# Kernel optimization log

Hardware: AMD Instinct MI355X
Metric: run time of the kernel (lower is better)

## Reference

```python
import jax, jax.numpy as jnp
import numpy as np

N_NODES, N_EDGES, N_GRAPHS, N_FEATS = 100000, 1600000, 256, 128
BN_EPS = 1e-5


def setup_inputs() -> dict:
    key = jax.random.key(0)
    ks = jax.random.split(key, 12)
    x = jax.random.normal(ks[0], (N_NODES, N_FEATS), jnp.float32)
    edge_index = jax.random.randint(ks[1], (2, N_EDGES), 0, N_NODES, dtype=jnp.int64)
    batch = jnp.sort(jax.random.randint(ks[2], (N_NODES,), 0, N_GRAPHS, dtype=jnp.int64))
    s = 0.05
    return {
        "x": x,
        "edge_index": edge_index,
        "batch": batch,
        "W1": jax.random.normal(ks[3], (N_FEATS, 32), jnp.float32) * s,
        "b1": jnp.zeros((32,), jnp.float32),
        "W2": jax.random.normal(ks[4], (32, 64), jnp.float32) * s,
        "b2": jnp.zeros((64,), jnp.float32),
        "fcW1": jax.random.normal(ks[5], (64, 32), jnp.float32) * s,
        "fcb1": jnp.zeros((32,), jnp.float32),
        "gamma": jnp.ones((32,), jnp.float32),
        "beta": jnp.zeros((32,), jnp.float32),
        "fcW2": jax.random.normal(ks[6], (32, 1), jnp.float32) * s,
        "fcb2": jnp.zeros((1,), jnp.float32),
    }


def _gcn_conv(x, src, dst, deg_inv, W, b):
    # PyG GCNConv: h = x @ W; out[d] = sum_e norm_e * h[src_e] + self-loop + b
    h = x @ W  # [N, out]
    norm = deg_inv[src] * deg_inv[dst]  # [E]
    msg = h[src] * norm[:, None]
    out = jax.ops.segment_sum(msg, dst, num_segments=x.shape[0])
    out = out + (deg_inv * deg_inv)[:, None] * h  # self-loop contribution
    return out + b


def reference(x, edge_index, batch, W1, b1, W2, b2, fcW1, fcb1, gamma, beta, fcW2, fcb2):
    src, dst = edge_index[0], edge_index[1]
    n = x.shape[0]
    # degree with self loops, computed on target nodes (PyG default)
    deg = 1.0 + jax.ops.segment_sum(jnp.ones_like(src, dtype=x.dtype), dst, num_segments=n)
    deg_inv = jax.lax.rsqrt(deg)
    h = _gcn_conv(x, src, dst, deg_inv, W1, b1)   # [N, 32]
    h = _gcn_conv(h, src, dst, deg_inv, W2, b2)   # [N, 64]
    # scatter_mean over graph batch
    sums = jax.ops.segment_sum(h, batch, num_segments=N_GRAPHS)  # [G, 64]
    cnt = jax.ops.segment_sum(jnp.ones((n,), h.dtype), batch, num_segments=N_GRAPHS)
    pooled = sums / jnp.maximum(cnt, 1.0)[:, None]
    # head: Linear -> ReLU -> BatchNorm1d (batch stats) -> Dropout(eval=id) -> Linear -> Softplus
    z = jax.nn.relu(pooled @ fcW1 + fcb1)  # [G, 32]
    mu = jnp.mean(z, axis=0)
    var = jnp.var(z, axis=0)
    z = (z - mu) * jax.lax.rsqrt(var + BN_EPS) * gamma + beta
    out = jax.nn.softplus(z @ fcW2 + fcb2)  # [G, 1]
    return out
```

## Files before the change

kernel.cpp:

```cpp
#include <hip/hip_runtime.h>

#define NN 100000
#define NE 1600000
#define NG 256

#define BSH 8
#define NPB 256
#define NBKT ((NN + NPB - 1) / NPB)
#define STRIDE 4608
#define TILE 8192
#define NB_P1 ((NE + TILE - 1) / TILE)

__device__ __forceinline__ unsigned short f2bf(float x) {
    unsigned int u = __float_as_uint(x);
    u += 0x7FFFu + ((u >> 16) & 1u);
    return (unsigned short)(u >> 16);
}
__device__ __forceinline__ float2 bf2x2(unsigned int v) {
    float2 r;
    r.x = __uint_as_float(v << 16);
    r.y = __uint_as_float(v & 0xFFFF0000u);
    return r;
}
__device__ __forceinline__ unsigned int bfpack(float x, float y) {
    return (unsigned int)f2bf(x) | ((unsigned int)f2bf(y) << 16);
}

__global__ __launch_bounds__(1024) void part_kernel(const int* __restrict__ src,
                                                    const int* __restrict__ dst,
                                                    int* __restrict__ bkt_cur,
                                                    int* __restrict__ epack) {
    __shared__ int hist[512];
    __shared__ int scan0[512];
    __shared__ int cur[NBKT];
    __shared__ int gbase[NBKT];
    __shared__ int stage[TILE];
    __shared__ unsigned short sb[TILE];
    int tid = threadIdx.x;
    int e0 = blockIdx.x * TILE;
    int e1 = min(e0 + TILE, NE);
    int n = e1 - e0;

    for (int i = tid; i < 512; i += 1024) hist[i] = 0;
    __syncthreads();

    int d_[8], s_[8];
#pragma unroll
    for (int k = 0; k < 8; ++k) {
        int e = e0 + tid + k * 1024;
        if (e < e1) {
            d_[k] = dst[e];
            s_[k] = src[e];
            atomicAdd(&hist[d_[k] >> BSH], 1);
        }
    }
    __syncthreads();

    if (tid < 512) scan0[tid] = hist[tid];
    __syncthreads();
    for (int off = 1; off < 512; off <<= 1) {
        int t = (tid < 512 && tid >= off) ? scan0[tid - off] : 0;
        __syncthreads();
        if (tid < 512) scan0[tid] += t;
        __syncthreads();
    }
    if (tid < NBKT) {
        int h = hist[tid];
        int ex = scan0[tid] - h;
        cur[tid] = ex;
        gbase[tid] = tid * STRIDE + (h ? atomicAdd(&bkt_cur[tid], h) : 0) - ex;
    }
    __syncthreads();

#pragma unroll
    for (int k = 0; k < 8; ++k) {
        int e = e0 + tid + k * 1024;
        if (e < e1) {
            int d = d_[k];
            int bk = d >> BSH;
            int p = atomicAdd(&cur[bk], 1);
            stage[p] = s_[k] | ((d & (NPB - 1)) << 17);
            sb[p] = (unsigned short)bk;
        }
    }
    __syncthreads();

    for (int j = tid; j < n; j += 1024) {
        int bk = sb[j];
        int a = gbase[bk] + j;
        if (a < (bk + 1) * STRIDE)
            epack[a] = stage[j];
    }
}

__global__ __launch_bounds__(512) void build_kernel(const int* __restrict__ epack,
                                                    const int* __restrict__ bkt_cur,
                                                    int* __restrict__ row_beg,
                                                    int* __restrict__ row_deg,
                                                    int* __restrict__ col,
                                                    float* __restrict__ deg_inv) {
    __shared__ int cnt[NPB];
    __shared__ int ts[NPB];
    int b = blockIdx.x;
    int tid = threadIdx.x;
    int ebase = b * STRIDE;
    int eend = ebase + min(bkt_cur[b], STRIDE);
    int nbase = b << BSH;
    if (tid < NPB) cnt[tid] = 0;
    __syncthreads();
    for (int e = ebase + tid; e < eend; e += 512)
        atomicAdd(&cnt[epack[e] >> 17], 1);
    __syncthreads();
    int v = 0;
    if (tid < NPB) {
        v = cnt[tid];
        ts[tid] = v;
    }
    __syncthreads();
    for (int off = 1; off < NPB; off <<= 1) {
        int t = (tid < NPB && tid >= off) ? ts[tid - off] : 0;
        __syncthreads();
        if (tid < NPB) ts[tid] += t;
        __syncthreads();
    }
    if (tid < NPB) {
        int loff = ts[tid] - v;
        int node = nbase + tid;
        if (node < NN) {
            row_beg[node] = ebase + loff;
            row_deg[node] = v;
            deg_inv[node] = rsqrtf(1.0f + (float)v);
        }
        cnt[tid] = loff;
    }
    __syncthreads();
    for (int e = ebase + tid; e < eend; e += 512) {
        int rec = epack[e];
        int r = atomicAdd(&cnt[rec >> 17], 1);
        col[ebase + r] = rec & 0x1FFFF;
    }
}

__global__ __launch_bounds__(256) void gemm_x_w1(const float* __restrict__ x,
                                                 const float* __restrict__ W,
                                                 const float* __restrict__ deg_inv,
                                                 unsigned short* __restrict__ h, int N) {
    __shared__ float wsh[128 * 32];
    __shared__ float xs[32][132];
    int tid = threadIdx.x;
    int row0 = blockIdx.x * 32;
    for (int i = tid; i < 1024; i += 256)
        ((float4*)wsh)[i] = ((const float4*)W)[i];
    for (int i = tid; i < 1024; i += 256) {
        int r = i >> 5, c4 = i & 31;
        *(float4*)&xs[r][c4 * 4] = ((const float4*)(x + (size_t)(row0 + r) * 128))[c4];
    }
    __syncthreads();
    int r = tid >> 3;
    int c8 = (tid & 7) * 4;
    float acc0 = 0.f, acc1 = 0.f, acc2 = 0.f, acc3 = 0.f;
#pragma unroll
    for (int k0 = 0; k0 < 128; k0 += 4) {
        float4 xv = *(const float4*)&xs[r][k0];
#pragma unroll
        for (int j = 0; j < 4; ++j) {
            float xk = (&xv.x)[j];
            float4 wv = *(const float4*)&wsh[(k0 + j) * 32 + c8];
            acc0 += xk * wv.x;
            acc1 += xk * wv.y;
            acc2 += xk * wv.z;
            acc3 += xk * wv.w;
        }
    }
    float di = deg_inv[row0 + r];
    ushort4 o;
    o.x = f2bf(acc0 * di);
    o.y = f2bf(acc1 * di);
    o.z = f2bf(acc2 * di);
    o.w = f2bf(acc3 * di);
    *(ushort4*)&h[(size_t)(row0 + r) * 32 + c8] = o;
}

template <int MODE>
__global__ __launch_bounds__(256) void conv_bf_kernel(const int* __restrict__ row_beg,
                                                      const int* __restrict__ row_deg,
                                                      const int* __restrict__ col,
                                                      const uint2* __restrict__ h2,
                                                      const float* __restrict__ deg_inv,
                                                      const float* __restrict__ b,
                                                      uint2* __restrict__ out_bf,
                                                      const int* __restrict__ batch,
                                                      float* __restrict__ gsum,
                                                      float* __restrict__ gcnt) {
    __shared__ float sacc[2][32];
    __shared__ float scnt[2];
    __shared__ int sg[2];
    int tid = threadIdx.x;
    int gid = blockIdx.x * 256 + tid;
    int node = gid >> 3;
    int L = gid & 7;
    if (MODE == 1) {
        if (tid < 64) sacc[tid >> 5][tid & 31] = 0.f;
        if (tid < 2) scnt[tid] = 0.f;
        if (tid == 0) {
            sg[0] = batch[(size_t)blockIdx.x * 32];
            sg[1] = batch[(size_t)blockIdx.x * 32 + 31];
        }
    }
    int beg = row_beg[node];
    int end = beg + row_deg[node];
    uint2 sv = h2[node * 8 + L];
    float2 s0 = bf2x2(sv.x), s1 = bf2x2(sv.y);
    float a00 = s0.x, a01 = s0.y, a02 = s1.x, a03 = s1.y;
    float a10 = 0.f, a11 = 0.f, a12 = 0.f, a13 = 0.f;
    float a20 = 0.f, a21 = 0.f, a22 = 0.f, a23 = 0.f;
    float a30 = 0.f, a31 = 0.f, a32 = 0.f, a33 = 0.f;
    for (int j0 = beg; j0 < end; j0 += 8) {
        int idx = j0 + L;
        int myc = (idx < end) ? col[idx] : 0;
        int m = end - j0;
        if (m > 8) m = 8;
        int t = 0;
        for (; t + 4 <= m; t += 4) {
            int c0 = __shfl(myc, t, 8);
            int c1 = __shfl(myc, t + 1, 8);
            int c2 = __shfl(myc, t + 2, 8);
            int c3 = __shfl(myc, t + 3, 8);
            uint2 v0 = h2[c0 * 8 + L];
            uint2 v1 = h2[c1 * 8 + L];
            uint2 v2 = h2[c2 * 8 + L];
            uint2 v3 = h2[c3 * 8 + L];
            float2 p0 = bf2x2(v0.x), q0 = bf2x2(v0.y);
            float2 p1 = bf2x2(v1.x), q1 = bf2x2(v1.y);
            float2 p2 = bf2x2(v2.x), q2 = bf2x2(v2.y);
            float2 p3 = bf2x2(v3.x), q3 = bf2x2(v3.y);
            a00 += p0.x; a01 += p0.y; a02 += q0.x; a03 += q0.y;
            a10 += p1.x; a11 += p1.y; a12 += q1.x; a13 += q1.y;
            a20 += p2.x; a21 += p2.y; a22 += q2.x; a23 += q2.y;
            a30 += p3.x; a31 += p3.y; a32 += q3.x; a33 += q3.y;
        }
        for (; t < m; ++t) {
            int c = __shfl(myc, t, 8);
            uint2 v = h2[c * 8 + L];
            float2 p = bf2x2(v.x), q = bf2x2(v.y);
            a00 += p.x; a01 += p.y; a02 += q.x; a03 += q.y;
        }
    }
    float c0 = (a00 + a10) + (a20 + a30);
    float c1 = (a01 + a11) + (a21 + a31);
    float c2 = (a02 + a12) + (a22 + a32);
    float c3 = (a03 + a13) + (a23 + a33);
    float di = deg_inv[node];
    if (MODE == 0) {
        float o0 = di * di * c0 + di * b[4 * L];
        float o1 = di * di * c1 + di * b[4 * L + 1];
        float o2 = di * di * c2 + di * b[4 * L + 2];
        float o3 = di * di * c3 + di * b[4 * L + 3];
        out_bf[node * 8 + L] = make_uint2(bfpack(o0, o1), bfpack(o2, o3));
    } else {
        float o0 = di * c0, o1 = di * c1, o2 = di * c2, o3 = di * c3;
        __syncthreads();
        int gn = batch[node];
        int base = 4 * L;
        if (gn == sg[0]) {
            atomicAdd(&sacc[0][base + 0], o0);
            atomicAdd(&sacc[0][base + 1], o1);
            atomicAdd(&sacc[0][base + 2], o2);
            atomicAdd(&sacc[0][base + 3], o3);
            if (L == 0) atomicAdd(&scnt[0], 1.f);
        } else if (gn == sg[1]) {
            atomicAdd(&sacc[1][base + 0], o0);
            atomicAdd(&sacc[1][base + 1], o1);
            atomicAdd(&sacc[1][base + 2], o2);
            atomicAdd(&sacc[1][base + 3], o3);
            if (L == 0) atomicAdd(&scnt[1], 1.f);
        } else {
            unsafeAtomicAdd(&gsum[gn * 32 + base + 0], o0);
            unsafeAtomicAdd(&gsum[gn * 32 + base + 1], o1);
            unsafeAtomicAdd(&gsum[gn * 32 + base + 2], o2);
            unsafeAtomicAdd(&gsum[gn * 32 + base + 3], o3);
            if (L == 0) unsafeAtomicAdd(&gcnt[gn], 1.f);
        }
        __syncthreads();
        if (tid < 64) {
            int s = tid >> 5, f = tid & 31;
            if (s == 0 || sg[1] != sg[0])
                unsafeAtomicAdd(&gsum[sg[s] * 32 + f], sacc[s][f]);
        }
        if (tid == 0) unsafeAtomicAdd(&gcnt[sg[0]], scnt[0]);
        if (tid == 1 && sg[1] != sg[0]) unsafeAtomicAdd(&gcnt[sg[1]], scnt[1]);
    }
}

__global__ __launch_bounds__(256) void head_kernel(const float* __restrict__ gsum,
                                                   const float* __restrict__ gcnt,
                                                   const float* __restrict__ W2,
                                                   const float* __restrict__ b2,
                                                   const float* __restrict__ fcW1,
                                                   const float* __restrict__ fcb1,
                                                   const float* __restrict__ gamma,
                                                   const float* __restrict__ beta,
                                                   const float* __restrict__ fcW2,
                                                   const float* __restrict__ fcb2,
                                                   float* __restrict__ out) {
    __shared__ float zs[NG][33];
    __shared__ float wcs[32 * 32];
    __shared__ float bcs[32];
    __shared__ float part1[8][32];
    __shared__ float part2[8][32];
    __shared__ float mu[32], rstd[32];
    int g = threadIdx.x;

    for (int idx = g; idx < 32 * 32; idx += 256) {
        int k = idx / 32, ch = idx % 32;
        float a = 0.f;
#pragma unroll
        for (int j = 0; j < 64; ++j) a += W2[k * 64 + j] * fcW1[j * 32 + ch];
        wcs[idx] = a;
    }
    if (g < 32) {
        float a = fcb1[g];
#pragma unroll
        for (int j = 0; j < 64; ++j) a += b2[j] * fcW1[j * 32 + g];
        bcs[g] = a;
    }
    __syncthreads();

    float p32[32];
    float inv = 1.0f / fmaxf(gcnt[g], 1.0f);
    {
        const float4* gs4 = (const float4*)(gsum + g * 32);
#pragma unroll
        for (int q = 0; q < 8; ++q) {
            float4 v = gs4[q];
            p32[q * 4 + 0] = v.x * inv;
            p32[q * 4 + 1] = v.y * inv;
            p32[q * 4 + 2] = v.z * inv;
            p32[q * 4 + 3] = v.w * inv;
        }
    }
#pragma unroll 4
    for (int ch = 0; ch < 32; ++ch) {
        float acc = bcs[ch];
#pragma unroll
        for (int k = 0; k < 32; ++k) acc += p32[k] * wcs[k * 32 + ch];
        zs[g][ch] = fmaxf(acc, 0.f);
    }
    __syncthreads();

    {
        int ch = g & 31, seg = g >> 5;
        float s = 0.f, sq = 0.f;
#pragma unroll
        for (int i = 0; i < 32; ++i) {
            float v = zs[seg * 32 + i][ch];
            s += v;
            sq += v * v;
        }
        part1[seg][ch] = s;
        part2[seg][ch] = sq;
    }
    __syncthreads();
    if (g < 32) {
        float s = 0.f, sq = 0.f;
#pragma unroll
        for (int i = 0; i < 8; ++i) { s += part1[i][g]; sq += part2[i][g]; }
        float m = s / NG;
        float v = sq / NG - m * m;
        mu[g] = m;
        rstd[g] = rsqrtf(fmaxf(v, 0.f) + 1e-5f);
    }
    __syncthreads();

    float acc = fcb2[0];
#pragma unroll 4
    for (int ch = 0; ch < 32; ++ch) {
        float zn = (zs[g][ch] - mu[ch]) * rstd[ch] * gamma[ch] + beta[ch];
        acc += zn * fcW2[ch];
    }
    out[g] = fmaxf(acc, 0.f) + log1pf(expf(-fabsf(acc)));
}

extern "C" void kernel_launch(void* const* d_in, const int* in_sizes, int n_in,
                              void* d_out, int out_size, void* d_ws, size_t ws_size,
                              hipStream_t stream) {
    const float* x     = (const float*)d_in[0];
    const int*   ei    = (const int*)d_in[1];
    const int*   batch = (const int*)d_in[2];
    const float* W1    = (const float*)d_in[3];
    const float* b1    = (const float*)d_in[4];
    const float* W2    = (const float*)d_in[5];
    const float* b2    = (const float*)d_in[6];
    const float* fcW1  = (const float*)d_in[7];
    const float* fcb1  = (const float*)d_in[8];
    const float* gamma = (const float*)d_in[9];
    const float* beta  = (const float*)d_in[10];
    const float* fcW2  = (const float*)d_in[11];
    const float* fcb2  = (const float*)d_in[12];
    float* out = (float*)d_out;

    char* p = (char*)d_ws;
    int*   bkt_cur = (int*)p;        p += 400 * 4;
    float* gsum    = (float*)p;      p += (size_t)NG * 32 * 4;
    float* gcnt    = (float*)p;      p += (size_t)NG * 4;
    float* deg_inv = (float*)p;      p += (size_t)NN * 4;
    int*   row_beg = (int*)p;        p += (size_t)(NN + 8) * 4;
    int*   row_deg = (int*)p;        p += (size_t)(NN + 8) * 4;
    int*   epack   = (int*)p;        p += (size_t)NBKT * STRIDE * 4;
    int*   col     = (int*)p;        p += (size_t)NBKT * STRIDE * 4;
    unsigned short* h1s = (unsigned short*)p;  p += (size_t)NN * 32 * 2;
    uint2*          t1  = (uint2*)p;           p += (size_t)NN * 8 * 8;

    const int* srcv = ei;
    const int* dstv = ei + NE;

    hipMemsetAsync(bkt_cur, 0, 400 * 4 + (size_t)NG * 32 * 4 + (size_t)NG * 4, stream);

    part_kernel<<<NB_P1, 1024, 0, stream>>>(srcv, dstv, bkt_cur, epack);
    build_kernel<<<NBKT, 512, 0, stream>>>(epack, bkt_cur, row_beg, row_deg, col, deg_inv);

    gemm_x_w1<<<NN / 32, 256, 0, stream>>>(x, W1, deg_inv, h1s, NN);
    conv_bf_kernel<0><<<((size_t)NN * 8 + 255) / 256, 256, 0, stream>>>(
        row_beg, row_deg, col, (const uint2*)h1s, deg_inv, b1, t1, nullptr, nullptr, nullptr);

    conv_bf_kernel<1><<<((size_t)NN * 8 + 255) / 256, 256, 0, stream>>>(
        row_beg, row_deg, col, (const uint2*)t1, deg_inv, b1, nullptr, batch, gsum, gcnt);

    head_kernel<<<1, 256, 0, stream>>>(gsum, gcnt, W2, b2, fcW1, fcb1, gamma, beta, fcW2, fcb2, out);
}
```

Baseline: 227.1 us.

## Replace CSR build and pull convolution with bucketed push aggregation in shared memory

Removes the build_kernel that sorted each destination bucket into CSR rows. Degrees now come from global atomics in the partition kernel, and each convolution runs one 1024-thread block per 256-node bucket, accumulating neighbor features into a shared-memory tile with LDS atomics. The block then applies the self-loop, normalization and bias. This saves a kernel launch and the col/row arrays, but relies on heavy shared-memory float atomics and on only about 391 blocks, which may underfill the GPU.

New measurement: 893.4 us. 3.93x slower.

```diff
diff --git a/kernel.cpp b/kernel.cpp
--- a/kernel.cpp
+++ b/kernel.cpp
@@ -29,7 +29,8 @@
 __global__ __launch_bounds__(1024) void part_kernel(const int* __restrict__ src,
                                                     const int* __restrict__ dst,
                                                     int* __restrict__ bkt_cur,
-                                                    int* __restrict__ epack) {
+                                                    int* __restrict__ epack,
+                                                    int* __restrict__ deg) {
     __shared__ int hist[512];
     __shared__ int scan0[512];
     __shared__ int cur[NBKT];
@@ -87,63 +88,17 @@
 
     for (int j = tid; j < n; j += 1024) {
         int bk = sb[j];
+        int rec = stage[j];
         int a = gbase[bk] + j;
         if (a < (bk + 1) * STRIDE)
-            epack[a] = stage[j];
-    }
-}
-
-__global__ __launch_bounds__(512) void build_kernel(const int* __restrict__ epack,
-                                                    const int* __restrict__ bkt_cur,
-                                                    int* __restrict__ row_beg,
-                                                    int* __restrict__ row_deg,
-                                                    int* __restrict__ col,
-                                                    float* __restrict__ deg_inv) {
-    __shared__ int cnt[NPB];
-    __shared__ int ts[NPB];
-    int b = blockIdx.x;
-    int tid = threadIdx.x;
-    int ebase = b * STRIDE;
-    int eend = ebase + min(bkt_cur[b], STRIDE);
-    int nbase = b << BSH;
-    if (tid < NPB) cnt[tid] = 0;
-    __syncthreads();
-    for (int e = ebase + tid; e < eend; e += 512)
-        atomicAdd(&cnt[epack[e] >> 17], 1);
-    __syncthreads();
-    int v = 0;
-    if (tid < NPB) {
-        v = cnt[tid];
-        ts[tid] = v;
-    }
-    __syncthreads();
-    for (int off = 1; off < NPB; off <<= 1) {
-        int t = (tid < NPB && tid >= off) ? ts[tid - off] : 0;
-        __syncthreads();
-        if (tid < NPB) ts[tid] += t;
-        __syncthreads();
-    }
-    if (tid < NPB) {
-        int loff = ts[tid] - v;
-        int node = nbase + tid;
-        if (node < NN) {
-            row_beg[node] = ebase + loff;
-            row_deg[node] = v;
-            deg_inv[node] = rsqrtf(1.0f + (float)v);
-        }
-        cnt[tid] = loff;
-    }
-    __syncthreads();
-    for (int e = ebase + tid; e < eend; e += 512) {
-        int rec = epack[e];
-        int r = atomicAdd(&cnt[rec >> 17], 1);
-        col[ebase + r] = rec & 0x1FFFF;
+            epack[a] = rec;
+        atomicAdd(&deg[(bk << BSH) + (rec >> 17)], 1);
     }
 }
 
 __global__ __launch_bounds__(256) void gemm_x_w1(const float* __restrict__ x,
                                                  const float* __restrict__ W,
-                                                 const float* __restrict__ deg_inv,
+                                                 const int* __restrict__ deg,
                                                  unsigned short* __restrict__ h, int N) {
     __shared__ float wsh[128 * 32];
     __shared__ float xs[32][132];
@@ -172,7 +127,7 @@
             acc3 += xk * wv.w;
         }
     }
-    float di = deg_inv[row0 + r];
+    float di = rsqrtf(1.0f + (float)deg[row0 + r]);
     ushort4 o;
     o.x = f2bf(acc0 * di);
     o.y = f2bf(acc1 * di);
@@ -182,105 +137,119 @@
 }
 
 template <int MODE>
-__global__ __launch_bounds__(256) void conv_bf_kernel(const int* __restrict__ row_beg,
-                                                      const int* __restrict__ row_deg,
-                                                      const int* __restrict__ col,
-                                                      const uint2* __restrict__ h2,
-                                                      const float* __restrict__ deg_inv,
-                                                      const float* __restrict__ b,
-                                                      uint2* __restrict__ out_bf,
-                                                      const int* __restrict__ batch,
-                                                      float* __restrict__ gsum,
-                                                      float* __restrict__ gcnt) {
+__global__ __launch_bounds__(1024) void push_conv(const int* __restrict__ epack,
+                                                  const int* __restrict__ bkt_cur,
+                                                  const uint2* __restrict__ h2,
+                                                  const int* __restrict__ deg,
+                                                  const float* __restrict__ bias,
+                                                  uint2* __restrict__ out_bf,
+                                                  const int* __restrict__ batch,
+                                                  float* __restrict__ gsum,
+                                                  float* __restrict__ gcnt) {
+    __shared__ float acc[NPB * 32];
     __shared__ float sacc[2][32];
     __shared__ float scnt[2];
     __shared__ int sg[2];
+    int bk = blockIdx.x;
     int tid = threadIdx.x;
-    int gid = blockIdx.x * 256 + tid;
-    int node = gid >> 3;
-    int L = gid & 7;
+    int ebase = bk * STRIDE;
+    int ecnt = min(bkt_cur[bk], STRIDE);
+    int nbase = bk << BSH;
+
+    for (int i = tid; i < NPB * 32; i += 1024) acc[i] = 0.f;
     if (MODE == 1) {
         if (tid < 64) sacc[tid >> 5][tid & 31] = 0.f;
         if (tid < 2) scnt[tid] = 0.f;
         if (tid == 0) {
-            sg[0] = batch[(size_t)blockIdx.x * 32];
-            sg[1] = batch[(size_t)blockIdx.x * 32 + 31];
-        }
-    }
-    int beg = row_beg[node];
-    int end = beg + row_deg[node];
-    uint2 sv = h2[node * 8 + L];
-    float2 s0 = bf2x2(sv.x), s1 = bf2x2(sv.y);
-    float a00 = s0.x, a01 = s0.y, a02 = s1.x, a03 = s1.y;
-    float a10 = 0.f, a11 = 0.f, a12 = 0.f, a13 = 0.f;
-    float a20 = 0.f, a21 = 0.f, a22 = 0.f, a23 = 0.f;
-    float a30 = 0.f, a31 = 0.f, a32 = 0.f, a33 = 0.f;
-    for (int j0 = beg; j0 < end; j0 += 8) {
-        int idx = j0 + L;
-        int myc = (idx < end) ? col[idx] : 0;
-        int m = end - j0;
-        if (m > 8) m = 8;
-        int t = 0;
-        for (; t + 4 <= m; t += 4) {
-            int c0 = __shfl(myc, t, 8);
-            int c1 = __shfl(myc, t + 1, 8);
-            int c2 = __shfl(myc, t + 2, 8);
-            int c3 = __shfl(myc, t + 3, 8);
-            uint2 v0 = h2[c0 * 8 + L];
-            uint2 v1 = h2[c1 * 8 + L];
-            uint2 v2 = h2[c2 * 8 + L];
-            uint2 v3 = h2[c3 * 8 + L];
-            float2 p0 = bf2x2(v0.x), q0 = bf2x2(v0.y);
-            float2 p1 = bf2x2(v1.x), q1 = bf2x2(v1.y);
-            float2 p2 = bf2x2(v2.x), q2 = bf2x2(v2.y);
-            float2 p3 = bf2x2(v3.x), q3 = bf2x2(v3.y);
-            a00 += p0.x; a01 += p0.y; a02 += q0.x; a03 += q0.y;
-            a10 += p1.x; a11 += p1.y; a12 += q1.x; a13 += q1.y;
-            a20 += p2.x; a21 += p2.y; a22 += q2.x; a23 += q2.y;
-            a30 += p3.x; a31 += p3.y; a32 += q3.x; a33 += q3.y;
-        }
-        for (; t < m; ++t) {
-            int c = __shfl(myc, t, 8);
-            uint2 v = h2[c * 8 + L];
-            float2 p = bf2x2(v.x), q = bf2x2(v.y);
-            a00 += p.x; a01 += p.y; a02 += q.x; a03 += q.y;
-        }
-    }
-    float c0 = (a00 + a10) + (a20 + a30);
-    float c1 = (a01 + a11) + (a21 + a31);
-    float c2 = (a02 + a12) + (a22 + a32);
-    float c3 = (a03 + a13) + (a23 + a33);
-    float di = deg_inv[node];
-    if (MODE == 0) {
-        float o0 = di * di * c0 + di * b[4 * L];
-        float o1 = di * di * c1 + di * b[4 * L + 1];
-        float o2 = di * di * c2 + di * b[4 * L + 2];
-        float o3 = di * di * c3 + di * b[4 * L + 3];
-        out_bf[node * 8 + L] = make_uint2(bfpack(o0, o1), bfpack(o2, o3));
-    } else {
-        float o0 = di * c0, o1 = di * c1, o2 = di * c2, o3 = di * c3;
-        __syncthreads();
-        int gn = batch[node];
-        int base = 4 * L;
-        if (gn == sg[0]) {
-            atomicAdd(&sacc[0][base + 0], o0);
-            atomicAdd(&sacc[0][base + 1], o1);
-            atomicAdd(&sacc[0][base + 2], o2);
-            atomicAdd(&sacc[0][base + 3], o3);
-            if (L == 0) atomicAdd(&scnt[0], 1.f);
-        } else if (gn == sg[1]) {
-            atomicAdd(&sacc[1][base + 0], o0);
-            atomicAdd(&sacc[1][base + 1], o1);
-            atomicAdd(&sacc[1][base + 2], o2);
-            atomicAdd(&sacc[1][base + 3], o3);
-            if (L == 0) atomicAdd(&scnt[1], 1.f);
+            sg[0] = batch[nbase];
+            sg[1] = batch[min(nbase + NPB - 1, NN - 1)];
+        }
+    }
+    __syncthreads();
+
+    int g = tid >> 3, L = tid & 7;
+    int e = g;
+    for (; e + 384 < ecnt; e += 512) {
+        int rec0 = epack[ebase + e];
+        int rec1 = epack[ebase + e + 128];
+        int rec2 = epack[ebase + e + 256];
+        int rec3 = epack[ebase + e + 384];
+        uint2 v0 = h2[(rec0 & 0x1FFFF) * 8 + L];
+        uint2 v1 = h2[(rec1 & 0x1FFFF) * 8 + L];
+        uint2 v2 = h2[(rec2 & 0x1FFFF) * 8 + L];
+        uint2 v3 = h2[(rec3 & 0x1FFFF) * 8 + L];
+        int l0 = rec0 >> 17, l1 = rec1 >> 17, l2 = rec2 >> 17, l3 = rec3 >> 17;
+        float2 p, q;
+        float* a0 = &acc[l0 * 32 + ((4 * (L + l0)) & 31)];
+        p = bf2x2(v0.x); q = bf2x2(v0.y);
+        atomicAdd(a0 + 0, p.x); atomicAdd(a0 + 1, p.y);
+        atomicAdd(a0 + 2, q.x); atomicAdd(a0 + 3, q.y);
+        float* a1 = &acc[l1 * 32 + ((4 * (L + l1)) & 31)];
+        p = bf2x2(v1.x); q = bf2x2(v1.y);
+        atomicAdd(a1 + 0, p.x); atomicAdd(a1 + 1, p.y);
+        atomicAdd(a1 + 2, q.x); atomicAdd(a1 + 3, q.y);
+        float* a2 = &acc[l2 * 32 + ((4 * (L + l2)) & 31)];
+        p = bf2x2(v2.x); q = bf2x2(v2.y);
+        atomicAdd(a2 + 0, p.x); atomicAdd(a2 + 1, p.y);
+        atomicAdd(a2 + 2, q.x); atomicAdd(a2 + 3, q.y);
+        float* a3 = &acc[l3 * 32 + ((4 * (L + l3)) & 31)];
+        p = bf2x2(v3.x); q = bf2x2(v3.y);
+        atomicAdd(a3 + 0, p.x); atomicAdd(a3 + 1, p.y);
+        atomicAdd(a3 + 2, q.x); atomicAdd(a3 + 3, q.y);
+    }
+    for (; e < ecnt; e += 128) {
+        int rec = epack[ebase + e];
+        uint2 v = h2[(rec & 0x1FFFF) * 8 + L];
+        int l = rec >> 17;
+        float2 p = bf2x2(v.x), q = bf2x2(v.y);
+        float* a = &acc[l * 32 + ((4 * (L + l)) & 31)];
+        atomicAdd(a + 0, p.x); atomicAdd(a + 1, p.y);
+        atomicAdd(a + 2, q.x); atomicAdd(a + 3, q.y);
+    }
+    __syncthreads();
+
+    for (int i = tid; i < NPB * 8; i += 1024) {
+        int local = i >> 3, Lf = i & 7;
+        int node = nbase + local;
+        if (node >= NN) continue;
+        float4 av = *(float4*)&acc[local * 32 + ((4 * (Lf + local)) & 31)];
+        uint2 sv = h2[(size_t)node * 8 + Lf];
+        float2 s0 = bf2x2(sv.x), s1 = bf2x2(sv.y);
+        float c0 = av.x + s0.x, c1 = av.y + s0.y;
+        float c2 = av.z + s1.x, c3 = av.w + s1.y;
+        float di = rsqrtf(1.0f + (float)deg[node]);
+        if (MODE == 0) {
+            float o0 = di * di * c0 + di * bias[4 * Lf + 0];
+            float o1 = di * di * c1 + di * bias[4 * Lf + 1];
+            float o2 = di * di * c2 + di * bias[4 * Lf + 2];
+            float o3 = di * di * c3 + di * bias[4 * Lf + 3];
+            out_bf[(size_t)node * 8 + Lf] = make_uint2(bfpack(o0, o1), bfpack(o2, o3));
         } else {
-            unsafeAtomicAdd(&gsum[gn * 32 + base + 0], o0);
-            unsafeAtomicAdd(&gsum[gn * 32 + base + 1], o1);
-            unsafeAtomicAdd(&gsum[gn * 32 + base + 2], o2);
-            unsafeAtomicAdd(&gsum[gn * 32 + base + 3], o3);
-            if (L == 0) unsafeAtomicAdd(&gcnt[gn], 1.f);
-        }
+            float o0 = di * c0, o1 = di * c1, o2 = di * c2, o3 = di * c3;
+            int gn = batch[node];
+            int fb = 4 * Lf;
+            if (gn == sg[0]) {
+                atomicAdd(&sacc[0][fb + 0], o0);
+                atomicAdd(&sacc[0][fb + 1], o1);
+                atomicAdd(&sacc[0][fb + 2], o2);
+                atomicAdd(&sacc[0][fb + 3], o3);
+                if (Lf == 0) atomicAdd(&scnt[0], 1.f);
+            } else if (gn == sg[1]) {
+                atomicAdd(&sacc[1][fb + 0], o0);
+                atomicAdd(&sacc[1][fb + 1], o1);
+                atomicAdd(&sacc[1][fb + 2], o2);
+                atomicAdd(&sacc[1][fb + 3], o3);
+                if (Lf == 0) atomicAdd(&scnt[1], 1.f);
+            } else {
+                unsafeAtomicAdd(&gsum[gn * 32 + fb + 0], o0);
+                unsafeAtomicAdd(&gsum[gn * 32 + fb + 1], o1);
+                unsafeAtomicAdd(&gsum[gn * 32 + fb + 2], o2);
+                unsafeAtomicAdd(&gsum[gn * 32 + fb + 3], o3);
+                if (Lf == 0) unsafeAtomicAdd(&gcnt[gn], 1.f);
+            }
+        }
+    }
+    if (MODE == 1) {
         __syncthreads();
         if (tid < 64) {
             int s = tid >> 5, f = tid & 31;
@@ -403,28 +372,25 @@
     int*   bkt_cur = (int*)p;        p += 400 * 4;
     float* gsum    = (float*)p;      p += (size_t)NG * 32 * 4;
     float* gcnt    = (float*)p;      p += (size_t)NG * 4;
-    float* deg_inv = (float*)p;      p += (size_t)NN * 4;
-    int*   row_beg = (int*)p;        p += (size_t)(NN + 8) * 4;
-    int*   row_deg = (int*)p;        p += (size_t)(NN + 8) * 4;
+    int*   deg     = (int*)p;        p += (size_t)NN * 4;
     int*   epack   = (int*)p;        p += (size_t)NBKT * STRIDE * 4;
-    int*   col     = (int*)p;        p += (size_t)NBKT * STRIDE * 4;
     unsigned short* h1s = (unsigned short*)p;  p += (size_t)NN * 32 * 2;
     uint2*          t1  = (uint2*)p;           p += (size_t)NN * 8 * 8;
 
     const int* srcv = ei;
     const int* dstv = ei + NE;
 
-    hipMemsetAsync(bkt_cur, 0, 400 * 4 + (size_t)NG * 32 * 4 + (size_t)NG * 4, stream);
-
-    part_kernel<<<NB_P1, 1024, 0, stream>>>(srcv, dstv, bkt_cur, epack);
-    build_kernel<<<NBKT, 512, 0, stream>>>(epack, bkt_cur, row_beg, row_deg, col, deg_inv);
-
-    gemm_x_w1<<<NN / 32, 256, 0, stream>>>(x, W1, deg_inv, h1s, NN);
-    conv_bf_kernel<0><<<((size_t)NN * 8 + 255) / 256, 256, 0, stream>>>(
-        row_beg, row_deg, col, (const uint2*)h1s, deg_inv, b1, t1, nullptr, nullptr, nullptr);
-
-    conv_bf_kernel<1><<<((size_t)NN * 8 + 255) / 256, 256, 0, stream>>>(
-        row_beg, row_deg, col, (const uint2*)t1, deg_inv, b1, nullptr, batch, gsum, gcnt);
+    hipMemsetAsync(bkt_cur, 0,
+                   400 * 4 + (size_t)NG * 32 * 4 + (size_t)NG * 4 + (size_t)NN * 4, stream);
+
+    part_kernel<<<NB_P1, 1024, 0, stream>>>(srcv, dstv, bkt_cur, epack, deg);
+
+    gemm_x_w1<<<NN / 32, 256, 0, stream>>>(x, W1, deg, h1s, NN);
+    push_conv<0><<<NBKT, 1024, 0, stream>>>(epack, bkt_cur, (const uint2*)h1s, deg, b1,
+                                            t1, nullptr, nullptr, nullptr);
+
+    push_conv<1><<<NBKT, 1024, 0, stream>>>(epack, bkt_cur, (const uint2*)t1, deg, b1,
+                                            nullptr, batch, gsum, gcnt);
 
     head_kernel<<<1, 256, 0, stream>>>(gsum, gcnt, W2, b2, fcW1, fcb1, gamma, beta, fcW2, fcb2, out);
 }
```
